# Kernel optimization log

Measured on AMD Instinct MI355X. Metric: run time of the kernel, lower is better.

## Reference

```python
import jax, jax.numpy as jnp
import numpy as np

N_NODES = 100000
N_HEDGES = 10000
D = 128  # i_d = v_d = e_d = q_d
NUM_CLASS = 10
E = 640000


def _linear_params(key, d_in, d_out):
    k1, k2 = jax.random.split(key)
    lim = 1.0 / np.sqrt(d_in)
    W = jax.random.uniform(k1, (d_in, d_out), jnp.float32, -lim, lim)
    b = jax.random.uniform(k2, (d_out,), jnp.float32, -lim, lim)
    return W, b


def setup_inputs() -> dict:
    key = jax.random.key(0)
    ks = jax.random.split(key, 12)
    vfeat = jax.random.normal(ks[0], (N_NODES, D), jnp.float32)
    efeat = jax.random.normal(ks[1], (N_HEDGES, D), jnp.float32)
    he_idx = jax.random.randint(ks[2], (E,), 0, N_HEDGES, jnp.int32)
    nd_idx = jax.random.randint(ks[3], (E,), 0, N_NODES, jnp.int32)
    Wfl, bfl = _linear_params(ks[4], D, D)   # first_layer_in: i_d -> v_d
    W1, b1 = _linear_params(ks[5], D, D)     # w1: e_d -> q_d
    W2, b2 = _linear_params(ks[6], D, D)     # w2: v_d -> q_d
    W3, b3 = _linear_params(ks[7], D, D)     # w3: v_d -> e_d
    W4, b4 = _linear_params(ks[8], D, D)     # w4: v_d -> q_d
    W5, b5 = _linear_params(ks[9], D, D)     # w5: e_d -> q_d
    W6, b6 = _linear_params(ks[10], D, D)    # w6: e_d -> v_d
    Wc, bc = _linear_params(ks[11], D, NUM_CLASS)
    return dict(vfeat=vfeat, efeat=efeat, he_idx=he_idx, nd_idx=nd_idx,
                first_layer=1, last_layer=1,
                Wfl=Wfl, bfl=bfl, W1=W1, b1=b1, W2=W2, b2=b2, W3=W3, b3=b3,
                W4=W4, b4=b4, W5=W5, b5=b5, W6=W6, b6=b6, Wc=Wc, bc=bc)


def _segment_softmax(logits, segs, num_segments):
    # softmax over the variable-size mailbox of each destination segment
    m = jax.ops.segment_max(logits, segs, num_segments=num_segments)
    m = jnp.where(jnp.isfinite(m), m, 0.0)  # empty segments
    e = jnp.exp(logits - m[segs])
    s = jax.ops.segment_sum(e, segs, num_segments=num_segments)
    return e / jnp.where(s > 0, s, 1.0)[segs]


def reference(vfeat, efeat, he_idx, nd_idx, first_layer, last_layer,
              Wfl, bfl, W1, b1, W2, b2, W3, b3, W4, b4, W5, b5, W6, b6, Wc, bc):
    scale = 1.0 / np.sqrt(D).astype(np.float32)
    # first_layer path (first_layer=1)
    feat_e = efeat @ Wfl + bfl                         # [M, v_d]
    k_e = feat_e @ W5 + b5                             # [M, q_d]
    v_e = feat_e @ W6 + b6                             # [M, v_d]
    q_v = vfeat @ W4 + b4                              # [N, q_d]
    # etype 'con': hyperedge -> node
    attn1 = jax.nn.leaky_relu((k_e[he_idx] * q_v[nd_idx]).sum(-1)) * scale  # [E]
    a1 = _segment_softmax(attn1, nd_idx, N_NODES)
    feat_v = jax.ops.segment_sum(a1[:, None] * v_e[he_idx], nd_idx,
                                 num_segments=N_NODES)  # [N, v_d]
    # etype 'in': node -> hyperedge
    k_v = feat_v @ W2 + b2                             # [N, q_d]
    v_v = feat_v @ W3 + b3                             # [N, e_d]
    q_e = feat_e @ W1 + b1                             # [M, q_d]
    attn2 = jax.nn.leaky_relu((k_v[nd_idx] * q_e[he_idx]).sum(-1)) * scale  # [E]
    a2 = _segment_softmax(attn2, he_idx, N_HEDGES)
    feat_e2 = jax.ops.segment_sum(a2[:, None] * v_v[nd_idx], he_idx,
                                  num_segments=N_HEDGES)  # [M, e_d]
    # last_layer path (last_layer=1): classification head (file save omitted)
    pred = feat_e2 @ Wc + bc                           # [M, num_class]
    return pred
```

## Files before the change

kernel.cpp:

```cpp
#include <hip/hip_runtime.h>
#include <hip/hip_bf16.h>
#include <math.h>


#define HY_M 10000
#define HY_N 100000
#define HY_E 640000

#define SH_N 9
#define NB_N 196
#define SH_M 6
#define NB_M 157

typedef float        f32x4 __attribute__((ext_vector_type(4)));
typedef unsigned int u32x4 __attribute__((ext_vector_type(4)));

__device__ __forceinline__ unsigned int f2bf(float x) {
    unsigned int u = __float_as_uint(x);
    return (u + 0x7fffu + ((u >> 16) & 1u)) >> 16;
}
__device__ __forceinline__ float2 bf2x2(unsigned int w) {
    float lo = __uint_as_float(w << 16);
    float hi = __uint_as_float(w & 0xffff0000u);
    return make_float2(lo, hi);
}
__device__ __forceinline__ float dot8(uint4 kw, float4 qa, float4 qb) {
    float2 k0 = bf2x2(kw.x), k1 = bf2x2(kw.y), k2 = bf2x2(kw.z), k3 = bf2x2(kw.w);
    return k0.x * qa.x + k0.y * qa.y + k1.x * qa.z + k1.y * qa.w
         + k2.x * qb.x + k2.y * qb.y + k3.x * qb.z + k3.y * qb.w;
}
__device__ __forceinline__ void unpack8(uint4 vw, float (&vf)[8]) {
    float2 v0 = bf2x2(vw.x), v1 = bf2x2(vw.y), v2 = bf2x2(vw.z), v3 = bf2x2(vw.w);
    vf[0] = v0.x; vf[1] = v0.y; vf[2] = v1.x; vf[3] = v1.y;
    vf[4] = v2.x; vf[5] = v2.y; vf[6] = v3.x; vf[7] = v3.y;
}

__global__ void zero_ints(int* __restrict__ p, int n) {
    int i = blockIdx.x * blockDim.x + threadIdx.x;
    if (i < n) p[i] = 0;
}

__launch_bounds__(256)
__global__ void coarse_hist(const int* __restrict__ nd, const int* __restrict__ he,
                            int* __restrict__ gcntN, int* __restrict__ gcntM, int E) {
    __shared__ int hN[256], hM[256];
    const int t = threadIdx.x;
    hN[t] = 0; hM[t] = 0;
    __syncthreads();
    const int base = blockIdx.x * 4096;
    for (int i = t; i < 4096; i += 256) {
        int e = base + i;
        if (e < E) {
            atomicAdd(&hN[nd[e] >> SH_N], 1);
            atomicAdd(&hM[he[e] >> SH_M], 1);
        }
    }
    __syncthreads();
    if (hN[t]) atomicAdd(&gcntN[t], hN[t]);
    if (hM[t]) atomicAdd(&gcntM[t], hM[t]);
}

__global__ void coarse_scan(const int* __restrict__ gcntN, const int* __restrict__ gcntM,
                            int* __restrict__ coffN, int* __restrict__ coffM, int E) {
    __shared__ int s[256];
    const int* g = blockIdx.x ? gcntM : gcntN;
    int* o = blockIdx.x ? coffM : coffN;
    const int nb = blockIdx.x ? NB_M : NB_N;
    const int t = threadIdx.x;
    int v = (t < nb) ? g[t] : 0;
    int orig = v;
    s[t] = v; __syncthreads();
    for (int off = 1; off < 256; off <<= 1) {
        int x = (t >= off) ? s[t - off] : 0;
        __syncthreads(); s[t] += x; __syncthreads();
    }
    if (t < nb) o[t] = s[t] - orig;
    if (t == 0) o[nb] = E;
}

__launch_bounds__(256)
__global__ void part_scatter(const int* __restrict__ nd, const int* __restrict__ he,
                             const int* __restrict__ coffN, const int* __restrict__ coffM,
                             int* __restrict__ gcurN, int* __restrict__ gcurM,
                             unsigned int* __restrict__ stN, unsigned int* __restrict__ stM,
                             int E) {
    __shared__ int hN[256], hM[256];
    const int t = threadIdx.x;
    hN[t] = 0; hM[t] = 0;
    __syncthreads();
    const int base = blockIdx.x * 4096;
    for (int i = t; i < 4096; i += 256) {
        int e = base + i;
        if (e < E) {
            atomicAdd(&hN[nd[e] >> SH_N], 1);
            atomicAdd(&hM[he[e] >> SH_M], 1);
        }
    }
    __syncthreads();
    int cN = hN[t], cM = hM[t];
    __syncthreads();
    if (cN) hN[t] = coffN[t] + atomicAdd(&gcurN[t], cN);
    if (cM) hM[t] = coffM[t] + atomicAdd(&gcurM[t], cM);
    __syncthreads();
    for (int i = t; i < 4096; i += 256) {
        int e = base + i;
        if (e < E) {
            int d = nd[e], h = he[e];
            int pN = atomicAdd(&hN[d >> SH_N], 1);
            stN[pN] = ((unsigned int)(d & 511) << 14) | (unsigned int)h;
            int pM = atomicAdd(&hM[h >> SH_M], 1);
            stM[pM] = ((unsigned int)(h & 63) << 17) | (unsigned int)d;
        }
    }
}

__launch_bounds__(256)
__global__ void bucket_build(const unsigned int* __restrict__ stN,
                             const unsigned int* __restrict__ stM,
                             const int* __restrict__ coffN, const int* __restrict__ coffM,
                             int* __restrict__ nd_off, int* __restrict__ he_off,
                             int* __restrict__ nd_adj, int* __restrict__ he_adj,
                             int* __restrict__ dcntg) {
    __shared__ int cnt[512];
    __shared__ int cur[512];
    __shared__ int ps[256];
    __shared__ int dh[64];
    int b = blockIdx.x;
    const int t = threadIdx.x;
    const unsigned int* st; const int* coff; int* offout; int* adj;
    int dmin, dcnt2, sshift; unsigned int smask; int ntot;
    const bool isN = b < NB_N;
    if (isN) {
        st = stN; coff = coffN; offout = nd_off; adj = nd_adj;
        dmin = b << SH_N; dcnt2 = min(512, HY_N - dmin);
        sshift = 14; smask = 0x3FFFu; ntot = HY_N;
    } else {
        b -= NB_N;
        st = stM; coff = coffM; offout = he_off; adj = he_adj;
        dmin = b << SH_M; dcnt2 = min(64, HY_M - dmin);
        sshift = 17; smask = 0x1FFFFu; ntot = HY_M;
    }
    const int cbase = coff[b], cend = coff[b + 1];
    cnt[t] = 0; cnt[t + 256] = 0;
    if (t < 64) dh[t] = 0;
    __syncthreads();
    for (int k = cbase + t; k < cend; k += 256)
        atomicAdd(&cnt[st[k] >> sshift], 1);
    __syncthreads();
    int a0 = cnt[2 * t], a1 = cnt[2 * t + 1];
    int pair = a0 + a1;
    ps[t] = pair;
    __syncthreads();
    for (int off = 1; off < 256; off <<= 1) {
        int x = (t >= off) ? ps[t - off] : 0;
        __syncthreads(); ps[t] += x; __syncthreads();
    }
    int excl = ps[t] - pair;
    cur[2 * t]     = cbase + excl;
    cur[2 * t + 1] = cbase + excl + a0;
    __syncthreads();
    for (int i = t; i < dcnt2; i += 256) offout[dmin + i] = cur[i];
    if (t == 0 && dmin + dcnt2 == ntot) offout[ntot] = cend;
    if (isN) {
        for (int i = t; i < dcnt2; i += 256)
            atomicAdd(&dh[min(cnt[i], 63)], 1);
    }
    __syncthreads();
    if (isN && t < 64 && dh[t]) atomicAdd(&dcntg[t], dh[t]);
    for (int k = cbase + t; k < cend; k += 256) {
        unsigned int w = st[k];
        int pos = atomicAdd(&cur[w >> sshift], 1);
        adj[pos] = (int)(w & smask);
    }
}

__global__ void deg_scan(const int* __restrict__ dcnt, int* __restrict__ dcur) {
    int t = threadIdx.x;
    int rt = 63 - t;
    int v = dcnt[rt];
    int s = v;
    for (int o = 1; o < 64; o <<= 1) {
        int x = __shfl_up(s, o, 64);
        if (t >= o) s += x;
    }
    dcur[rt] = s - v;
}

__launch_bounds__(256)
__global__ void deg_scatter(const int* __restrict__ off, int* __restrict__ dcur,
                            int* __restrict__ nperm, int n) {
    __shared__ int h[64];
    __shared__ int basev[64];
    int t = threadIdx.x;
    if (t < 64) h[t] = 0;
    __syncthreads();
    int i = blockIdx.x * blockDim.x + t;
    int bin = 0, lpos = 0;
    bool valid = i < n;
    if (valid) {
        bin = min(off[i + 1] - off[i], 63);
        lpos = atomicAdd(&h[bin], 1);
    }
    __syncthreads();
    if (t < 64 && h[t]) basev[t] = atomicAdd(&dcur[t], h[t]);
    __syncthreads();
    if (valid) nperm[basev[bin] + lpos] = i;
}

__device__ __forceinline__ void gemm_accum(const float* __restrict__ A,
        const float* __restrict__ W, int nrows, float* wlds,
        float (&acc)[4][4], int row0) {
    const int tid = threadIdx.x;
    const int cg = tid & 31;
    for (int i = tid; i < 4096; i += 512)
        ((float4*)wlds)[i] = ((const float4*)W)[i];
    __syncthreads();
    const float4* A0 = (const float4*)(A + (size_t)min(row0 + 0, nrows - 1) * 128);
    const float4* A1 = (const float4*)(A + (size_t)min(row0 + 1, nrows - 1) * 128);
    const float4* A2 = (const float4*)(A + (size_t)min(row0 + 2, nrows - 1) * 128);
    const float4* A3 = (const float4*)(A + (size_t)min(row0 + 3, nrows - 1) * 128);
    #pragma unroll 2
    for (int kq = 0; kq < 32; ++kq) {
        float4 ar[4] = {A0[kq], A1[kq], A2[kq], A3[kq]};
        const float4* wk = (const float4*)(wlds + kq * 512);
        float4 wr[4] = {wk[cg], wk[32 + cg], wk[64 + cg], wk[96 + cg]};
        #pragma unroll
        for (int r = 0; r < 4; ++r) {
            float av[4] = {ar[r].x, ar[r].y, ar[r].z, ar[r].w};
            #pragma unroll
            for (int j = 0; j < 4; ++j) {
                float wv[4] = {wr[j].x, wr[j].y, wr[j].z, wr[j].w};
                #pragma unroll
                for (int c = 0; c < 4; ++c)
                    acc[r][c] = fmaf(av[j], wv[c], acc[r][c]);
            }
        }
    }
}

__device__ __forceinline__ void gemm_store_f32(const float* __restrict__ b,
        float* __restrict__ Cf, int nrows, float (&acc)[4][4], int row0) {
    const int cg = threadIdx.x & 31;
    const float4 bv = ((const float4*)b)[cg];
    #pragma unroll
    for (int r = 0; r < 4; ++r) {
        int gr = row0 + r;
        if (gr < nrows) {
            float4 o = {acc[r][0] + bv.x, acc[r][1] + bv.y,
                        acc[r][2] + bv.z, acc[r][3] + bv.w};
            ((float4*)(Cf + (size_t)gr * 128))[cg] = o;
        }
    }
}

__launch_bounds__(512)
__global__ void gemm_pair(const float* __restrict__ Aa, const float* __restrict__ Wa,
                          float* __restrict__ Ca,
                          const float* __restrict__ Ab, const float* __restrict__ Wb,
                          float* __restrict__ Cb2, const float* __restrict__ zb) {
    __shared__ __align__(16) float wlds[16384];
    const int rs = threadIdx.x >> 5;
    const int row0 = blockIdx.x * 64 + rs * 4;
    const float* A = blockIdx.y ? Ab : Aa;
    const float* W = blockIdx.y ? Wb : Wa;
    float* C = blockIdx.y ? Cb2 : Ca;
    float acc[4][4] = {};
    gemm_accum(A, W, 128, wlds, acc, row0);
    gemm_store_f32(zb, C, 128, acc, row0);
}

__launch_bounds__(512)
__global__ void gemm_trip(const float* __restrict__ Wfl, const float* __restrict__ bfl,
        const float* __restrict__ W54, const float* __restrict__ b54v,
        const float* __restrict__ W6, const float* __restrict__ b6,
        const float* __restrict__ W12, const float* __restrict__ b12v,
        const float* __restrict__ w1b2, const float* __restrict__ s12,
        const float* __restrict__ w5b4, const float* __restrict__ s54,
        float* __restrict__ Wk, float* __restrict__ Wv, float* __restrict__ Wq,
        float* __restrict__ bk, float* __restrict__ bv, float* __restrict__ bq,
        float* __restrict__ u_c, float* __restrict__ u_k,
        float* __restrict__ t_c, float* __restrict__ t_k,
        const float* __restrict__ zb) {
    __shared__ __align__(16) float wlds[16384];
    const int y = blockIdx.y;
    if (y == 3) {
        if (blockIdx.x != 0) return;
        int t = threadIdx.x;
        if (t < 128) {
            float a1 = 0.f, a2 = 0.f, a3 = 0.f;
            for (int j = 0; j < 128; ++j) {
                float f = bfl[j];
                a1 += f * W54[j * 128 + t];
                a2 += f * W6[j * 128 + t];
                a3 += f * W12[j * 128 + t];
            }
            bk[t] = a1 + b54v[t];
            bv[t] = a2 + b6[t];
            bq[t] = a3 + b12v[t];
        } else if (t < 256) {
            int k = t - 128;
            float a1 = 0.f, a2 = 0.f;
            for (int j = 0; j < 128; ++j) {
                float f = Wfl[k * 128 + j];
                a1 += f * w1b2[j];
                a2 += f * w5b4[j];
            }
            u_c[k] = a1;
            u_k[k] = a2;
        }
        if (t == 0) {
            float a1 = 0.f, a2 = 0.f;
            for (int j = 0; j < 128; ++j) {
                a1 += bfl[j] * w1b2[j];
                a2 += bfl[j] * w5b4[j];
            }
            *t_c = a1 + *s12;
            *t_k = a2 + *s54;
        }
        return;
    }
    const int rs = threadIdx.x >> 5;
    const int row0 = blockIdx.x * 64 + rs * 4;
    const float* W = y == 0 ? W54 : (y == 1 ? W6 : W12);
    float* C = y == 0 ? Wk : (y == 1 ? Wv : Wq);
    float acc[4][4] = {};
    gemm_accum(Wfl, W, 128, wlds, acc, row0);
    gemm_store_f32(zb, C, 128, acc, row0);
}

__launch_bounds__(256)
__global__ void gemm_m(const float* __restrict__ A,
        const float* __restrict__ Wk, const float* __restrict__ bk,
        const float* __restrict__ Wv, const float* __restrict__ bvv,
        const float* __restrict__ Wq, const float* __restrict__ bq,
        unsigned short* __restrict__ kv, float* __restrict__ qt, int nrows) {
    __shared__ __align__(16) float wlds[128 * 64];
    const int tid = threadIdx.x;
    const int mat = blockIdx.y >> 1;
    const int half = blockIdx.y & 1;
    const float* W = mat == 0 ? Wk : (mat == 1 ? Wv : Wq);
    const float* bb = mat == 0 ? bk : (mat == 1 ? bvv : bq);
    const float4* W4 = (const float4*)W;
    float4* wl4 = (float4*)wlds;
    for (int i = tid; i < 2048; i += 256)
        wl4[i] = W4[(i >> 4) * 32 + half * 16 + (i & 15)];
    __syncthreads();
    const int cg = tid & 15;
    const int rs = tid >> 4;
    const int row0 = blockIdx.x * 32 + rs * 2;
    const float4* A0 = (const float4*)(A + (size_t)min(row0, nrows - 1) * 128);
    const float4* A1 = (const float4*)(A + (size_t)min(row0 + 1, nrows - 1) * 128);
    float acc[2][4] = {};
    #pragma unroll 4
    for (int kq = 0; kq < 32; ++kq) {
        float4 a0 = A0[kq], a1 = A1[kq];
        float av0[4] = {a0.x, a0.y, a0.z, a0.w};
        float av1[4] = {a1.x, a1.y, a1.z, a1.w};
        #pragma unroll
        for (int jj = 0; jj < 4; ++jj) {
            float4 w4 = wl4[(4 * kq + jj) * 16 + cg];
            float wv4[4] = {w4.x, w4.y, w4.z, w4.w};
            #pragma unroll
            for (int c = 0; c < 4; ++c) {
                acc[0][c] = fmaf(av0[jj], wv4[c], acc[0][c]);
                acc[1][c] = fmaf(av1[jj], wv4[c], acc[1][c]);
            }
        }
    }
    const float4 bv4 = ((const float4*)bb)[half * 16 + cg];
    #pragma unroll
    for (int r = 0; r < 2; ++r) {
        int gr = row0 + r;
        if (gr < nrows) {
            float o0 = acc[r][0] + bv4.x, o1 = acc[r][1] + bv4.y;
            float o2 = acc[r][2] + bv4.z, o3 = acc[r][3] + bv4.w;
            if (mat == 2) {
                float4 o = {o0, o1, o2, o3};
                ((float4*)(qt + (size_t)gr * 128))[half * 16 + cg] = o;
            } else {
                uint2 pk;
                pk.x = f2bf(o0) | (f2bf(o1) << 16);
                pk.y = f2bf(o2) | (f2bf(o3) << 16);
                *(uint2*)(kv + (size_t)gr * 256 + mat * 128 + half * 64 + cg * 4) = pk;
            }
        }
    }
}

__device__ __forceinline__ void prep_vecs_body(const float* WX, const float* WY,
        const float* bX, const float* bY, float* bXY, float* wXbY, float* sXY, int t) {
    if (t < 128) {
        float acc = 0.f;
        for (int j = 0; j < 128; ++j) acc += WY[t * 128 + j] * bX[j];
        bXY[t] = acc;
    } else {
        int k = t - 128;
        float acc = 0.f;
        for (int j = 0; j < 128; ++j) acc += WX[k * 128 + j] * bY[j];
        wXbY[k] = acc;
    }
    if (t == 0) {
        float acc = 0.f;
        for (int j = 0; j < 128; ++j) acc += bX[j] * bY[j];
        *sXY = acc;
    }
}

__global__ void prep_a(const float* __restrict__ W1, const float* __restrict__ b1,
                       const float* __restrict__ W2, const float* __restrict__ b2,
                       const float* __restrict__ W3, const float* __restrict__ b3,
                       const float* __restrict__ W4, const float* __restrict__ b4,
                       const float* __restrict__ W5, const float* __restrict__ b5,
                       const float* __restrict__ Wc,
                       float* __restrict__ W2T, float* __restrict__ W4T,
                       float* __restrict__ b12v, float* __restrict__ w1b2,
                       float* __restrict__ s12,
                       float* __restrict__ b54v, float* __restrict__ w5b4,
                       float* __restrict__ s54,
                       float* __restrict__ W3c, float* __restrict__ b3c,
                       float* __restrict__ zeros) {
    const int x = blockIdx.x, t = threadIdx.x;
    if (x < 64) {
        int i = x * 256 + t;
        W2T[(i & 127) * 128 + (i >> 7)] = W2[i];
    } else if (x < 128) {
        int i = (x - 64) * 256 + t;
        W4T[(i & 127) * 128 + (i >> 7)] = W4[i];
    } else if (x == 128) {
        prep_vecs_body(W1, W2, b1, b2, b12v, w1b2, s12, t);
    } else if (x == 129) {
        prep_vecs_body(W5, W4, b5, b4, b54v, w5b4, s54, t);
    } else if (x < 136) {
        int i = (x - 130) * 256 + t;
        if (i < 1280) {
            int k = i / 10, c = i % 10;
            float acc = 0.f;
            for (int j = 0; j < 128; ++j) acc += W3[k * 128 + j] * Wc[j * 10 + c];
            W3c[i] = acc;
        } else if (i < 1290) {
            int c = i - 1280;
            float acc = 0.f;
            for (int j = 0; j < 128; ++j) acc += b3[j] * Wc[j * 10 + c];
            b3c[c] = acc;
        }
    } else {
        if (t < 128) zeros[t] = 0.f;
    }
}

__launch_bounds__(256)
__global__ void dotc2(const float* __restrict__ X,
                      const float* __restrict__ u1, const float* __restrict__ t1v,
                      const float* __restrict__ u2, const float* __restrict__ t2v,
                      float* __restrict__ o1, float* __restrict__ o2, int M) {
    int w = (blockIdx.x * blockDim.x + threadIdx.x) >> 6;
    int lane = threadIdx.x & 63;
    if (w >= M) return;
    float2 r = ((const float2*)(X + (size_t)w * 128))[lane];
    float2 a1 = ((const float2*)u1)[lane];
    float2 a2 = ((const float2*)u2)[lane];
    float d1 = r.x * a1.x + r.y * a1.y;
    float d2 = r.x * a2.x + r.y * a2.y;
    #pragma unroll
    for (int o = 32; o; o >>= 1) {
        d1 += __shfl_xor(d1, o, 64);
        d2 += __shfl_xor(d2, o, 64);
    }
    if (lane == 0) { o1[w] = d1 + *t1v; o2[w] = d2 + *t2v; }
}

__launch_bounds__(256)
__global__ void attn_s1(const float* __restrict__ vf,
                        const unsigned int* __restrict__ kv,
                        const float* __restrict__ ck,
                        const int* __restrict__ off, const int* __restrict__ adj,
                        const int* __restrict__ nperm,
                        unsigned int* __restrict__ fv,
                        int nseg, float scale) {
    int slot = (blockIdx.x * blockDim.x + threadIdx.x) >> 4;
    int j = threadIdx.x & 15;
    if (slot >= nseg) return;
    int seg = nperm[slot];
    int beg = off[seg], end = off[seg + 1];
    const f32x4* qp = (const f32x4*)(vf + (size_t)seg * 128 + 8 * j);
    f32x4 qa4 = __builtin_nontemporal_load(qp);
    f32x4 qb4 = __builtin_nontemporal_load(qp + 1);
    float4 qa = {qa4.x, qa4.y, qa4.z, qa4.w};
    float4 qb = {qb4.x, qb4.y, qb4.z, qb4.w};
    float m = -INFINITY, l = 0.f;
    float a[8] = {};
    int i = beg;
    const int cnt = end - beg;
    if (cnt >= 2) {
        int s0 = adj[i], s1 = adj[i + 1];
        uint4 kw0 = ((const uint4*)(kv + (size_t)s0 * 128))[j];
        uint4 vw0 = ((const uint4*)(kv + (size_t)s0 * 128 + 64))[j];
        float c0 = ck[s0];
        uint4 kw1 = ((const uint4*)(kv + (size_t)s1 * 128))[j];
        uint4 vw1 = ((const uint4*)(kv + (size_t)s1 * 128 + 64))[j];
        float c1 = ck[s1];
        for (; i + 1 < end; i += 2) {
            uint4 ka = kw0, va = vw0, kb = kw1, vb = vw1;
            float ca = c0, cb = c1;
            if (i + 3 < end) {
                int t0 = adj[i + 2], t1 = adj[i + 3];
                kw0 = ((const uint4*)(kv + (size_t)t0 * 128))[j];
                vw0 = ((const uint4*)(kv + (size_t)t0 * 128 + 64))[j];
                c0 = ck[t0];
                kw1 = ((const uint4*)(kv + (size_t)t1 * 128))[j];
                vw1 = ((const uint4*)(kv + (size_t)t1 * 128 + 64))[j];
                c1 = ck[t1];
            } else if (i + 2 < end) {
                int t0 = adj[i + 2];
                kw0 = ((const uint4*)(kv + (size_t)t0 * 128))[j];
                vw0 = ((const uint4*)(kv + (size_t)t0 * 128 + 64))[j];
                c0 = ck[t0];
            }
            float d1 = dot8(ka, qa, qb);
            float d2 = dot8(kb, qa, qb);
            d1 += __shfl_xor(d1, 8); d2 += __shfl_xor(d2, 8);
            d1 += __shfl_xor(d1, 4); d2 += __shfl_xor(d2, 4);
            d1 += __shfl_xor(d1, 2); d2 += __shfl_xor(d2, 2);
            d1 += __shfl_xor(d1, 1); d2 += __shfl_xor(d2, 1);
            d1 += ca; d2 += cb;
            d1 = (d1 >= 0.f ? d1 : 0.01f * d1) * scale;
            d2 = (d2 >= 0.f ? d2 : 0.01f * d2) * scale;
            float mn = fmaxf(fmaxf(m, d1), d2);
            float r  = __expf(m - mn);
            float p1 = __expf(d1 - mn);
            float p2 = __expf(d2 - mn);
            l = l * r + p1 + p2;
            float v1[8], v2[8];
            unpack8(va, v1); unpack8(vb, v2);
            #pragma unroll
            for (int t = 0; t < 8; ++t)
                a[t] = fmaf(p2, v2[t], fmaf(p1, v1[t], a[t] * r));
            m = mn;
        }
        if (i < end) {
            float d = dot8(kw0, qa, qb);
            d += __shfl_xor(d, 8); d += __shfl_xor(d, 4);
            d += __shfl_xor(d, 2); d += __shfl_xor(d, 1);
            d += c0;
            d = (d >= 0.f ? d : 0.01f * d) * scale;
            float mn = fmaxf(m, d);
            float r = __expf(m - mn);
            float p = __expf(d - mn);
            l = l * r + p;
            float v1[8]; unpack8(vw0, v1);
            #pragma unroll
            for (int t = 0; t < 8; ++t)
                a[t] = fmaf(p, v1[t], a[t] * r);
            m = mn;
        }
    } else if (cnt == 1) {
        int s0 = adj[i];
        uint4 kw0 = ((const uint4*)(kv + (size_t)s0 * 128))[j];
        uint4 vw0 = ((const uint4*)(kv + (size_t)s0 * 128 + 64))[j];
        float d = dot8(kw0, qa, qb);
        d += __shfl_xor(d, 8); d += __shfl_xor(d, 4);
        d += __shfl_xor(d, 2); d += __shfl_xor(d, 1);
        d += ck[s0];
        d = (d >= 0.f ? d : 0.01f * d) * scale;
        l = 1.f;
        float v1[8]; unpack8(vw0, v1);
        #pragma unroll
        for (int t = 0; t < 8; ++t) a[t] = v1[t];
    }
    float inv = (l > 0.f) ? 1.f / l : 0.f;
    u32x4 o;
    o.x = f2bf(a[0] * inv) | (f2bf(a[1] * inv) << 16);
    o.y = f2bf(a[2] * inv) | (f2bf(a[3] * inv) << 16);
    o.z = f2bf(a[4] * inv) | (f2bf(a[5] * inv) << 16);
    o.w = f2bf(a[6] * inv) | (f2bf(a[7] * inv) << 16);
    __builtin_nontemporal_store(o, (u32x4*)(fv + (size_t)seg * 64 + 4 * j));
}

__launch_bounds__(256)
__global__ void attn_s2(const float* __restrict__ QT, const float* __restrict__ cvec,
                        const unsigned int* __restrict__ fv,
                        const int* __restrict__ off, const int* __restrict__ adj,
                        float* __restrict__ agg, float* __restrict__ flag, float scale) {
    __shared__ float sm[16], sl[16];
    __shared__ float sacc[16][16][9];
    const int seg = blockIdx.x;
    const int g = threadIdx.x >> 4;
    const int j = threadIdx.x & 15;
    const int beg = off[seg], end = off[seg + 1];
    const f32x4* qp = (const f32x4*)(QT + (size_t)seg * 128 + 8 * j);
    f32x4 qa4 = __builtin_nontemporal_load(qp);
    f32x4 qb4 = __builtin_nontemporal_load(qp + 1);
    float4 qa = {qa4.x, qa4.y, qa4.z, qa4.w};
    float4 qb = {qb4.x, qb4.y, qb4.z, qb4.w};
    const float cadd = cvec[seg];
    float m = -INFINITY, l = 0.f;
    float a[8] = {};
    int it = beg + g;
    if (it + 16 < end) {
        int s0 = adj[it], s1 = adj[it + 16];
        uint4 rw0 = ((const uint4*)(fv + (size_t)s0 * 64))[j];
        uint4 rw1 = ((const uint4*)(fv + (size_t)s1 * 64))[j];
        for (; it + 16 < end; it += 32) {
            uint4 ra = rw0, rb = rw1;
            if (it + 48 < end) {
                int t0 = adj[it + 32], t1 = adj[it + 48];
                rw0 = ((const uint4*)(fv + (size_t)t0 * 64))[j];
                rw1 = ((const uint4*)(fv + (size_t)t1 * 64))[j];
            } else if (it + 32 < end) {
                int t0 = adj[it + 32];
                rw0 = ((const uint4*)(fv + (size_t)t0 * 64))[j];
            }
            float v1[8], v2[8];
            unpack8(ra, v1); unpack8(rb, v2);
            float d1 = v1[0] * qa.x + v1[1] * qa.y + v1[2] * qa.z + v1[3] * qa.w
                     + v1[4] * qb.x + v1[5] * qb.y + v1[6] * qb.z + v1[7] * qb.w;
            float d2 = v2[0] * qa.x + v2[1] * qa.y + v2[2] * qa.z + v2[3] * qa.w
                     + v2[4] * qb.x + v2[5] * qb.y + v2[6] * qb.z + v2[7] * qb.w;
            d1 += __shfl_xor(d1, 8); d2 += __shfl_xor(d2, 8);
            d1 += __shfl_xor(d1, 4); d2 += __shfl_xor(d2, 4);
            d1 += __shfl_xor(d1, 2); d2 += __shfl_xor(d2, 2);
            d1 += __shfl_xor(d1, 1); d2 += __shfl_xor(d2, 1);
            d1 += cadd; d2 += cadd;
            d1 = (d1 >= 0.f ? d1 : 0.01f * d1) * scale;
            d2 = (d2 >= 0.f ? d2 : 0.01f * d2) * scale;
            float mn = fmaxf(fmaxf(m, d1), d2);
            float r  = __expf(m - mn);
            float p1 = __expf(d1 - mn);
            float p2 = __expf(d2 - mn);
            l = l * r + p1 + p2;
            #pragma unroll
            for (int t = 0; t < 8; ++t)
                a[t] = fmaf(p2, v2[t], fmaf(p1, v1[t], a[t] * r));
            m = mn;
        }
        if (it < end) {
            float v1[8]; unpack8(rw0, v1);
            float d = v1[0] * qa.x + v1[1] * qa.y + v1[2] * qa.z + v1[3] * qa.w
                    + v1[4] * qb.x + v1[5] * qb.y + v1[6] * qb.z + v1[7] * qb.w;
            d += __shfl_xor(d, 8); d += __shfl_xor(d, 4);
            d += __shfl_xor(d, 2); d += __shfl_xor(d, 1);
            d += cadd;
            d = (d >= 0.f ? d : 0.01f * d) * scale;
            float mn = fmaxf(m, d);
            float r = __expf(m - mn);
            float p = __expf(d - mn);
            l = l * r + p;
            #pragma unroll
            for (int t = 0; t < 8; ++t) a[t] = fmaf(p, v1[t], a[t] * r);
            m = mn;
        }
    } else if (it < end) {
        int s0 = adj[it];
        uint4 rw0 = ((const uint4*)(fv + (size_t)s0 * 64))[j];
        float v1[8]; unpack8(rw0, v1);
        float d = v1[0] * qa.x + v1[1] * qa.y + v1[2] * qa.z + v1[3] * qa.w
                + v1[4] * qb.x + v1[5] * qb.y + v1[6] * qb.z + v1[7] * qb.w;
        d += __shfl_xor(d, 8); d += __shfl_xor(d, 4);
        d += __shfl_xor(d, 2); d += __shfl_xor(d, 1);
        d += cadd;
        d = (d >= 0.f ? d : 0.01f * d) * scale;
        m = d; l = 1.f;
        #pragma unroll
        for (int t = 0; t < 8; ++t) a[t] = v1[t];
    }
    if (j == 0) { sm[g] = m; sl[g] = l; }
    #pragma unroll
    for (int t = 0; t < 8; ++t) sacc[g][j][t] = a[t];
    __syncthreads();
    if (threadIdx.x < 16) {
        float M2 = -INFINITY;
        #pragma unroll 4
        for (int gg = 0; gg < 16; ++gg) if (sl[gg] > 0.f) M2 = fmaxf(M2, sm[gg]);
        float L = 0.f;
        float acc[8] = {};
        #pragma unroll 4
        for (int gg = 0; gg < 16; ++gg) {
            float f = (sl[gg] > 0.f) ? __expf(sm[gg] - M2) : 0.f;
            L += f * sl[gg];
            #pragma unroll
            for (int t = 0; t < 8; ++t) acc[t] += f * sacc[gg][threadIdx.x][t];
        }
        float inv = (L > 0.f) ? 1.f / L : 0.f;
        f32x4 o1 = {acc[0] * inv, acc[1] * inv, acc[2] * inv, acc[3] * inv};
        f32x4 o2 = {acc[4] * inv, acc[5] * inv, acc[6] * inv, acc[7] * inv};
        f32x4* op = (f32x4*)(agg + (size_t)seg * 128 + 8 * threadIdx.x);
        __builtin_nontemporal_store(o1, op);
        __builtin_nontemporal_store(o2, op + 1);
        if (threadIdx.x == 0) flag[seg] = (L > 0.f) ? 1.f : 0.f;
    }
}

__global__ void head2(const float* __restrict__ agg, const float* __restrict__ flag,
                      const float* __restrict__ W3c, const float* __restrict__ b3c,
                      const float* __restrict__ bc, float* __restrict__ out, int M) {
    int t = blockIdx.x * blockDim.x + threadIdx.x;
    if (t >= M * 10) return;
    int row = t / 10, c = t % 10;
    float acc = bc[c] + flag[row] * b3c[c];
    #pragma unroll 8
    for (int k = 0; k < 128; ++k)
        acc = fmaf(agg[(size_t)row * 128 + k], W3c[k * 10 + c], acc);
    out[t] = acc;
}

extern "C" void kernel_launch(void* const* d_in, const int* in_sizes, int n_in,
                              void* d_out, int out_size, void* d_ws, size_t ws_size,
                              hipStream_t stream) {
    const float* vfeat = (const float*)d_in[0];
    const float* efeat = (const float*)d_in[1];
    const int*   he    = (const int*)d_in[2];
    const int*   nd    = (const int*)d_in[3];
    const float* Wfl = (const float*)d_in[6],  *bfl = (const float*)d_in[7];
    const float* W1  = (const float*)d_in[8],  *b1  = (const float*)d_in[9];
    const float* W2  = (const float*)d_in[10], *b2  = (const float*)d_in[11];
    const float* W3  = (const float*)d_in[12], *b3  = (const float*)d_in[13];
    const float* W4  = (const float*)d_in[14], *b4  = (const float*)d_in[15];
    const float* W5  = (const float*)d_in[16], *b5  = (const float*)d_in[17];
    const float* W6  = (const float*)d_in[18], *b6  = (const float*)d_in[19];
    const float* Wc  = (const float*)d_in[20], *bc  = (const float*)d_in[21];
    float* out = (float*)d_out;
    float* ws  = (float*)d_ws;

    const int M = HY_M, N = HY_N, E = HY_E;

    float* qt_e  = ws + 0;
    float* agg   = ws + 1280000;
    float* c_e   = ws + 2560000;
    float* ck    = ws + 2570000;
    float* flag  = ws + 2580000;
    float* W2T   = ws + 2590000;
    float* W4T   = ws + 2606384;
    float* W12   = ws + 2622768;
    float* W54   = ws + 2639152;
    float* Wk    = ws + 2655536;
    float* Wv    = ws + 2671920;
    float* Wq    = ws + 2688304;
    float* W3c   = ws + 2704688;
    float* b3c   = ws + 2705968;
    float* b12v  = ws + 2705984;
    float* w1b2  = ws + 2706112;
    float* s12   = ws + 2706240;
    float* b54v  = ws + 2706244;
    float* w5b4  = ws + 2706372;
    float* s54   = ws + 2706500;
    float* bk    = ws + 2706504;
    float* bv    = ws + 2706632;
    float* bq    = ws + 2706760;
    float* u_c   = ws + 2706888;
    float* u_k   = ws + 2707016;
    float* t_c   = ws + 2707144;
    float* t_k   = ws + 2707148;
    float* zeros = ws + 2707152;
    unsigned int* kv_bf = (unsigned int*)(ws + 2707280);
    unsigned int* fv_bf = kv_bf + (size_t)M * 128;
    int* nd_off = (int*)(fv_bf + (size_t)N * 64);
    int* he_off = nd_off + 100001;
    int* nd_adj = he_off + 10001;
    int* he_adj = nd_adj + 640000;
    int* nperm  = he_adj + 640000;
    unsigned int* stN = (unsigned int*)(nperm + 100000);
    unsigned int* stM = stN + 640000;
    int* gcntN = (int*)(stM + 640000);
    int* gcntM = gcntN + 256;
    int* gcurN = gcntM + 256;
    int* gcurM = gcurN + 256;
    int* dcnt  = gcurM + 256;
    int* dcur  = dcnt + 64;
    int* coffN = dcur + 64;
    int* coffM = coffN + 256;

    const float scale = 0.08838834764831843f;
    const int nchunk = (E + 4095) / 4096;

    zero_ints<<<5, 256, 0, stream>>>(gcntN, 1152);
    coarse_hist<<<nchunk, 256, 0, stream>>>(nd, he, gcntN, gcntM, E);
    coarse_scan<<<2, 256, 0, stream>>>(gcntN, gcntM, coffN, coffM, E);
    part_scatter<<<nchunk, 256, 0, stream>>>(nd, he, coffN, coffM,
                                             gcurN, gcurM, stN, stM, E);
    bucket_build<<<NB_N + NB_M, 256, 0, stream>>>(stN, stM, coffN, coffM,
                                                  nd_off, he_off, nd_adj, he_adj,
                                                  dcnt);
    deg_scan<<<1, 64, 0, stream>>>(dcnt, dcur);
    deg_scatter<<<(N + 255) / 256, 256, 0, stream>>>(nd_off, dcur, nperm, N);

    prep_a<<<137, 256, 0, stream>>>(W1, b1, W2, b2, W3, b3, W4, b4, W5, b5, Wc,
                                    W2T, W4T, b12v, w1b2, s12, b54v, w5b4, s54,
                                    W3c, b3c, zeros);
    gemm_pair<<<dim3(2, 2), 512, 0, stream>>>(W1, W2T, W12, W5, W4T, W54, zeros);
    gemm_trip<<<dim3(2, 4), 512, 0, stream>>>(Wfl, bfl, W54, b54v, W6, b6, W12, b12v,
                                              w1b2, s12, w5b4, s54,
                                              Wk, Wv, Wq, bk, bv, bq,
                                              u_c, u_k, t_c, t_k, zeros);

    gemm_m<<<dim3((M + 31) / 32, 6), 256, 0, stream>>>(
        efeat, Wk, bk, Wv, bv, Wq, bq, (unsigned short*)kv_bf, qt_e, M);
    dotc2<<<(M * 64 + 255) / 256, 256, 0, stream>>>(efeat, u_c, t_c, u_k, t_k,
                                                    c_e, ck, M);

    attn_s1<<<(N * 16 + 255) / 256, 256, 0, stream>>>(
        vfeat, kv_bf, ck, nd_off, nd_adj, nperm, fv_bf, N, scale);

    attn_s2<<<M, 256, 0, stream>>>(qt_e, c_e, fv_bf, he_off, he_adj, agg, flag, scale);

    head2<<<(M * 10 + 255) / 256, 256, 0, stream>>>(agg, flag, W3c, b3c, bc, out, M);
}
```

Before: 212.8 us.

## Fuse small kernels, shrink partition chunks, and unroll node attention by four

Several independent changes land together. The zeroing kernel is folded into prep_a, which now runs first. The dotc2 row-dot kernel becomes an extra grid slice of gemm_m, and the head classifier is fused into the attn_s2 epilogue, so the agg/flag buffers and two launches disappear. The histogram and scatter chunk size drops from 4096 to 1024 edges to get more blocks, and attn_s1 switches from a two-wide prefetching loop to a four-wide batched gather loop. These cut launch overhead and intermediate memory traffic, at the cost of more global atomics and losing the explicit software prefetch.

```diff
diff --git a/kernel.cpp b/kernel.cpp
--- a/kernel.cpp
+++ b/kernel.cpp
@@ -34,10 +34,10 @@
     vf[0] = v0.x; vf[1] = v0.y; vf[2] = v1.x; vf[3] = v1.y;
     vf[4] = v2.x; vf[5] = v2.y; vf[6] = v3.x; vf[7] = v3.y;
 }
-
-__global__ void zero_ints(int* __restrict__ p, int n) {
-    int i = blockIdx.x * blockDim.x + threadIdx.x;
-    if (i < n) p[i] = 0;
+__device__ __forceinline__ float red16(float d) {
+    d += __shfl_xor(d, 8); d += __shfl_xor(d, 4);
+    d += __shfl_xor(d, 2); d += __shfl_xor(d, 1);
+    return d;
 }
 
 __launch_bounds__(256)
@@ -47,8 +47,8 @@
     const int t = threadIdx.x;
     hN[t] = 0; hM[t] = 0;
     __syncthreads();
-    const int base = blockIdx.x * 4096;
-    for (int i = t; i < 4096; i += 256) {
+    const int base = blockIdx.x * 1024;
+    for (int i = t; i < 1024; i += 256) {
         int e = base + i;
         if (e < E) {
             atomicAdd(&hN[nd[e] >> SH_N], 1);
@@ -88,8 +88,8 @@
     const int t = threadIdx.x;
     hN[t] = 0; hM[t] = 0;
     __syncthreads();
-    const int base = blockIdx.x * 4096;
-    for (int i = t; i < 4096; i += 256) {
+    const int base = blockIdx.x * 1024;
+    for (int i = t; i < 1024; i += 256) {
         int e = base + i;
         if (e < E) {
             atomicAdd(&hN[nd[e] >> SH_N], 1);
@@ -102,7 +102,7 @@
     if (cN) hN[t] = coffN[t] + atomicAdd(&gcurN[t], cN);
     if (cM) hM[t] = coffM[t] + atomicAdd(&gcurM[t], cM);
     __syncthreads();
-    for (int i = t; i < 4096; i += 256) {
+    for (int i = t; i < 1024; i += 256) {
         int e = base + i;
         if (e < E) {
             int d = nd[e], h = he[e];
@@ -333,9 +333,32 @@
         const float* __restrict__ Wk, const float* __restrict__ bk,
         const float* __restrict__ Wv, const float* __restrict__ bvv,
         const float* __restrict__ Wq, const float* __restrict__ bq,
+        const float* __restrict__ u_c, const float* __restrict__ t_c,
+        const float* __restrict__ u_k, const float* __restrict__ t_k,
+        float* __restrict__ c_e, float* __restrict__ ck,
         unsigned short* __restrict__ kv, float* __restrict__ qt, int nrows) {
     __shared__ __align__(16) float wlds[128 * 64];
     const int tid = threadIdx.x;
+    if (blockIdx.y == 6) {
+        const int w = tid >> 6, lane = tid & 63;
+        float2 a1 = ((const float2*)u_c)[lane];
+        float2 a2 = ((const float2*)u_k)[lane];
+        for (int it = 0; it < 8; ++it) {
+            int row = blockIdx.x * 32 + it * 4 + w;
+            if (row < nrows) {
+                float2 r = ((const float2*)(A + (size_t)row * 128))[lane];
+                float d1 = r.x * a1.x + r.y * a1.y;
+                float d2 = r.x * a2.x + r.y * a2.y;
+                #pragma unroll
+                for (int o = 32; o; o >>= 1) {
+                    d1 += __shfl_xor(d1, o, 64);
+                    d2 += __shfl_xor(d2, o, 64);
+                }
+                if (lane == 0) { c_e[row] = d1 + *t_c; ck[row] = d2 + *t_k; }
+            }
+        }
+        return;
+    }
     const int mat = blockIdx.y >> 1;
     const int half = blockIdx.y & 1;
     const float* W = mat == 0 ? Wk : (mat == 1 ? Wv : Wq);
@@ -418,7 +441,7 @@
                        float* __restrict__ b54v, float* __restrict__ w5b4,
                        float* __restrict__ s54,
                        float* __restrict__ W3c, float* __restrict__ b3c,
-                       float* __restrict__ zeros) {
+                       float* __restrict__ zeros, int* __restrict__ zint) {
     const int x = blockIdx.x, t = threadIdx.x;
     if (x < 64) {
         int i = x * 256 + t;
@@ -443,30 +466,12 @@
             for (int j = 0; j < 128; ++j) acc += b3[j] * Wc[j * 10 + c];
             b3c[c] = acc;
         }
+    } else if (x == 136) {
+        if (t < 128) zeros[t] = 0.f;
     } else {
-        if (t < 128) zeros[t] = 0.f;
-    }
-}
-
-__launch_bounds__(256)
-__global__ void dotc2(const float* __restrict__ X,
-                      const float* __restrict__ u1, const float* __restrict__ t1v,
-                      const float* __restrict__ u2, const float* __restrict__ t2v,
-                      float* __restrict__ o1, float* __restrict__ o2, int M) {
-    int w = (blockIdx.x * blockDim.x + threadIdx.x) >> 6;
-    int lane = threadIdx.x & 63;
-    if (w >= M) return;
-    float2 r = ((const float2*)(X + (size_t)w * 128))[lane];
-    float2 a1 = ((const float2*)u1)[lane];
-    float2 a2 = ((const float2*)u2)[lane];
-    float d1 = r.x * a1.x + r.y * a1.y;
-    float d2 = r.x * a2.x + r.y * a2.y;
-    #pragma unroll
-    for (int o = 32; o; o >>= 1) {
-        d1 += __shfl_xor(d1, o, 64);
-        d2 += __shfl_xor(d2, o, 64);
-    }
-    if (lane == 0) { o1[w] = d1 + *t1v; o2[w] = d2 + *t2v; }
+        int i = (x - 137) * 256 + t;
+        if (i < 1152) zint[i] = 0;
+    }
 }
 
 __launch_bounds__(256)
@@ -490,82 +495,56 @@
     float m = -INFINITY, l = 0.f;
     float a[8] = {};
     int i = beg;
-    const int cnt = end - beg;
-    if (cnt >= 2) {
-        int s0 = adj[i], s1 = adj[i + 1];
-        uint4 kw0 = ((const uint4*)(kv + (size_t)s0 * 128))[j];
-        uint4 vw0 = ((const uint4*)(kv + (size_t)s0 * 128 + 64))[j];
-        float c0 = ck[s0];
-        uint4 kw1 = ((const uint4*)(kv + (size_t)s1 * 128))[j];
-        uint4 vw1 = ((const uint4*)(kv + (size_t)s1 * 128 + 64))[j];
-        float c1 = ck[s1];
-        for (; i + 1 < end; i += 2) {
-            uint4 ka = kw0, va = vw0, kb = kw1, vb = vw1;
-            float ca = c0, cb = c1;
-            if (i + 3 < end) {
-                int t0 = adj[i + 2], t1 = adj[i + 3];
-                kw0 = ((const uint4*)(kv + (size_t)t0 * 128))[j];
-                vw0 = ((const uint4*)(kv + (size_t)t0 * 128 + 64))[j];
-                c0 = ck[t0];
-                kw1 = ((const uint4*)(kv + (size_t)t1 * 128))[j];
-                vw1 = ((const uint4*)(kv + (size_t)t1 * 128 + 64))[j];
-                c1 = ck[t1];
-            } else if (i + 2 < end) {
-                int t0 = adj[i + 2];
-                kw0 = ((const uint4*)(kv + (size_t)t0 * 128))[j];
-                vw0 = ((const uint4*)(kv + (size_t)t0 * 128 + 64))[j];
-                c0 = ck[t0];
-            }
-            float d1 = dot8(ka, qa, qb);
-            float d2 = dot8(kb, qa, qb);
-            d1 += __shfl_xor(d1, 8); d2 += __shfl_xor(d2, 8);
-            d1 += __shfl_xor(d1, 4); d2 += __shfl_xor(d2, 4);
-            d1 += __shfl_xor(d1, 2); d2 += __shfl_xor(d2, 2);
-            d1 += __shfl_xor(d1, 1); d2 += __shfl_xor(d2, 1);
-            d1 += ca; d2 += cb;
-            d1 = (d1 >= 0.f ? d1 : 0.01f * d1) * scale;
-            d2 = (d2 >= 0.f ? d2 : 0.01f * d2) * scale;
-            float mn = fmaxf(fmaxf(m, d1), d2);
-            float r  = __expf(m - mn);
-            float p1 = __expf(d1 - mn);
-            float p2 = __expf(d2 - mn);
-            l = l * r + p1 + p2;
-            float v1[8], v2[8];
-            unpack8(va, v1); unpack8(vb, v2);
-            #pragma unroll
-            for (int t = 0; t < 8; ++t)
-                a[t] = fmaf(p2, v2[t], fmaf(p1, v1[t], a[t] * r));
-            m = mn;
-        }
-        if (i < end) {
-            float d = dot8(kw0, qa, qb);
-            d += __shfl_xor(d, 8); d += __shfl_xor(d, 4);
-            d += __shfl_xor(d, 2); d += __shfl_xor(d, 1);
-            d += c0;
-            d = (d >= 0.f ? d : 0.01f * d) * scale;
-            float mn = fmaxf(m, d);
-            float r = __expf(m - mn);
-            float p = __expf(d - mn);
-            l = l * r + p;
-            float v1[8]; unpack8(vw0, v1);
-            #pragma unroll
-            for (int t = 0; t < 8; ++t)
-                a[t] = fmaf(p, v1[t], a[t] * r);
-            m = mn;
-        }
-    } else if (cnt == 1) {
+    for (; i + 3 < end; i += 4) {
+        int s0 = adj[i], s1 = adj[i + 1], s2 = adj[i + 2], s3 = adj[i + 3];
+        const uint4* r0 = (const uint4*)(kv + (size_t)s0 * 128);
+        const uint4* r1 = (const uint4*)(kv + (size_t)s1 * 128);
+        const uint4* r2 = (const uint4*)(kv + (size_t)s2 * 128);
+        const uint4* r3 = (const uint4*)(kv + (size_t)s3 * 128);
+        uint4 k0 = r0[j], k1 = r1[j], k2 = r2[j], k3 = r3[j];
+        uint4 v0 = r0[16 + j], v1 = r1[16 + j], v2 = r2[16 + j], v3 = r3[16 + j];
+        float c0 = ck[s0], c1 = ck[s1], c2 = ck[s2], c3 = ck[s3];
+        float d0 = dot8(k0, qa, qb), d1 = dot8(k1, qa, qb);
+        float d2 = dot8(k2, qa, qb), d3 = dot8(k3, qa, qb);
+        #pragma unroll
+        for (int o = 8; o; o >>= 1) {
+            d0 += __shfl_xor(d0, o); d1 += __shfl_xor(d1, o);
+            d2 += __shfl_xor(d2, o); d3 += __shfl_xor(d3, o);
+        }
+        d0 += c0; d1 += c1; d2 += c2; d3 += c3;
+        d0 = (d0 >= 0.f ? d0 : 0.01f * d0) * scale;
+        d1 = (d1 >= 0.f ? d1 : 0.01f * d1) * scale;
+        d2 = (d2 >= 0.f ? d2 : 0.01f * d2) * scale;
+        d3 = (d3 >= 0.f ? d3 : 0.01f * d3) * scale;
+        float mn = fmaxf(fmaxf(fmaxf(d0, d1), fmaxf(d2, d3)), m);
+        float r  = __expf(m - mn);
+        float p0 = __expf(d0 - mn), p1 = __expf(d1 - mn);
+        float p2 = __expf(d2 - mn), p3 = __expf(d3 - mn);
+        l = l * r + p0 + p1 + p2 + p3;
+        float w0[8], w1[8], w2[8], w3[8];
+        unpack8(v0, w0); unpack8(v1, w1); unpack8(v2, w2); unpack8(v3, w3);
+        #pragma unroll
+        for (int t = 0; t < 8; ++t)
+            a[t] = fmaf(p3, w3[t], fmaf(p2, w2[t],
+                   fmaf(p1, w1[t], fmaf(p0, w0[t], a[t] * r))));
+        m = mn;
+    }
+    for (; i < end; ++i) {
         int s0 = adj[i];
-        uint4 kw0 = ((const uint4*)(kv + (size_t)s0 * 128))[j];
-        uint4 vw0 = ((const uint4*)(kv + (size_t)s0 * 128 + 64))[j];
-        float d = dot8(kw0, qa, qb);
-        d += __shfl_xor(d, 8); d += __shfl_xor(d, 4);
-        d += __shfl_xor(d, 2); d += __shfl_xor(d, 1);
+        const uint4* r0 = (const uint4*)(kv + (size_t)s0 * 128);
+        uint4 k0 = r0[j], v0 = r0[16 + j];
+        float d = dot8(k0, qa, qb);
+        d = red16(d);
         d += ck[s0];
         d = (d >= 0.f ? d : 0.01f * d) * scale;
-        l = 1.f;
-        float v1[8]; unpack8(vw0, v1);
-        #pragma unroll
-        for (int t = 0; t < 8; ++t) a[t] = v1[t];
+        float mn = fmaxf(m, d);
+        float r = __expf(m - mn);
+        float p = __expf(d - mn);
+        l = l * r + p;
+        float w0[8]; unpack8(v0, w0);
+        #pragma unroll
+        for (int t = 0; t < 8; ++t) a[t] = fmaf(p, w0[t], a[t] * r);
+        m = mn;
     }
     float inv = (l > 0.f) ? 1.f / l : 0.f;
     u32x4 o;
@@ -580,7 +559,9 @@
 __global__ void attn_s2(const float* __restrict__ QT, const float* __restrict__ cvec,
                         const unsigned int* __restrict__ fv,
                         const int* __restrict__ off, const int* __restrict__ adj,
-                        float* __restrict__ agg, float* __restrict__ flag, float scale) {
+                        const float* __restrict__ W3c, const float* __restrict__ b3c,
+                        const float* __restrict__ bc, float* __restrict__ out,
+                        float scale) {
     __shared__ float sm[16], sl[16];
     __shared__ float sacc[16][16][9];
     const int seg = blockIdx.x;
@@ -616,10 +597,8 @@
                      + v1[4] * qb.x + v1[5] * qb.y + v1[6] * qb.z + v1[7] * qb.w;
             float d2 = v2[0] * qa.x + v2[1] * qa.y + v2[2] * qa.z + v2[3] * qa.w
                      + v2[4] * qb.x + v2[5] * qb.y + v2[6] * qb.z + v2[7] * qb.w;
-            d1 += __shfl_xor(d1, 8); d2 += __shfl_xor(d2, 8);
-            d1 += __shfl_xor(d1, 4); d2 += __shfl_xor(d2, 4);
-            d1 += __shfl_xor(d1, 2); d2 += __shfl_xor(d2, 2);
-            d1 += __shfl_xor(d1, 1); d2 += __shfl_xor(d2, 1);
+            #pragma unroll
+            for (int o = 8; o; o >>= 1) { d1 += __shfl_xor(d1, o); d2 += __shfl_xor(d2, o); }
             d1 += cadd; d2 += cadd;
             d1 = (d1 >= 0.f ? d1 : 0.01f * d1) * scale;
             d2 = (d2 >= 0.f ? d2 : 0.01f * d2) * scale;
@@ -637,8 +616,7 @@
             float v1[8]; unpack8(rw0, v1);
             float d = v1[0] * qa.x + v1[1] * qa.y + v1[2] * qa.z + v1[3] * qa.w
                     + v1[4] * qb.x + v1[5] * qb.y + v1[6] * qb.z + v1[7] * qb.w;
-            d += __shfl_xor(d, 8); d += __shfl_xor(d, 4);
-            d += __shfl_xor(d, 2); d += __shfl_xor(d, 1);
+            d = red16(d);
             d += cadd;
             d = (d >= 0.f ? d : 0.01f * d) * scale;
             float mn = fmaxf(m, d);
@@ -655,8 +633,7 @@
         float v1[8]; unpack8(rw0, v1);
         float d = v1[0] * qa.x + v1[1] * qa.y + v1[2] * qa.z + v1[3] * qa.w
                 + v1[4] * qb.x + v1[5] * qb.y + v1[6] * qb.z + v1[7] * qb.w;
-        d += __shfl_xor(d, 8); d += __shfl_xor(d, 4);
-        d += __shfl_xor(d, 2); d += __shfl_xor(d, 1);
+        d = red16(d);
         d += cadd;
         d = (d >= 0.f ? d : 0.01f * d) * scale;
         m = d; l = 1.f;
@@ -668,6 +645,7 @@
     for (int t = 0; t < 8; ++t) sacc[g][j][t] = a[t];
     __syncthreads();
     if (threadIdx.x < 16) {
+        const int t16 = threadIdx.x;
         float M2 = -INFINITY;
         #pragma unroll 4
         for (int gg = 0; gg < 16; ++gg) if (sl[gg] > 0.f) M2 = fmaxf(M2, sm[gg]);
@@ -678,29 +656,32 @@
             float f = (sl[gg] > 0.f) ? __expf(sm[gg] - M2) : 0.f;
             L += f * sl[gg];
             #pragma unroll
-            for (int t = 0; t < 8; ++t) acc[t] += f * sacc[gg][threadIdx.x][t];
+            for (int t = 0; t < 8; ++t) acc[t] += f * sacc[gg][t16][t];
         }
         float inv = (L > 0.f) ? 1.f / L : 0.f;
-        f32x4 o1 = {acc[0] * inv, acc[1] * inv, acc[2] * inv, acc[3] * inv};
-        f32x4 o2 = {acc[4] * inv, acc[5] * inv, acc[6] * inv, acc[7] * inv};
-        f32x4* op = (f32x4*)(agg + (size_t)seg * 128 + 8 * threadIdx.x);
-        __builtin_nontemporal_store(o1, op);
-        __builtin_nontemporal_store(o2, op + 1);
-        if (threadIdx.x == 0) flag[seg] = (L > 0.f) ? 1.f : 0.f;
-    }
-}
-
-__global__ void head2(const float* __restrict__ agg, const float* __restrict__ flag,
-                      const float* __restrict__ W3c, const float* __restrict__ b3c,
-                      const float* __restrict__ bc, float* __restrict__ out, int M) {
-    int t = blockIdx.x * blockDim.x + threadIdx.x;
-    if (t >= M * 10) return;
-    int row = t / 10, c = t % 10;
-    float acc = bc[c] + flag[row] * b3c[c];
-    #pragma unroll 8
-    for (int k = 0; k < 128; ++k)
-        acc = fmaf(agg[(size_t)row * 128 + k], W3c[k * 10 + c], acc);
-    out[t] = acc;
+        float fl  = (L > 0.f) ? 1.f : 0.f;
+        #pragma unroll
+        for (int t = 0; t < 8; ++t) acc[t] *= inv;
+        float pp[10];
+        #pragma unroll
+        for (int c = 0; c < 10; ++c) {
+            float s = 0.f;
+            #pragma unroll
+            for (int t = 0; t < 8; ++t)
+                s = fmaf(acc[t], W3c[(8 * t16 + t) * 10 + c], s);
+            pp[c] = s;
+        }
+        #pragma unroll
+        for (int o = 8; o; o >>= 1) {
+            #pragma unroll
+            for (int c = 0; c < 10; ++c) pp[c] += __shfl_xor(pp[c], o);
+        }
+        if (t16 == 0) {
+            #pragma unroll
+            for (int c = 0; c < 10; ++c)
+                out[(size_t)seg * 10 + c] = pp[c] + fl * b3c[c] + bc[c];
+        }
+    }
 }
 
 extern "C" void kernel_launch(void* const* d_in, const int* in_sizes, int n_in,
@@ -724,34 +705,32 @@
     const int M = HY_M, N = HY_N, E = HY_E;
 
     float* qt_e  = ws + 0;
-    float* agg   = ws + 1280000;
-    float* c_e   = ws + 2560000;
-    float* ck    = ws + 2570000;
-    float* flag  = ws + 2580000;
-    float* W2T   = ws + 2590000;
-    float* W4T   = ws + 2606384;
-    float* W12   = ws + 2622768;
-    float* W54   = ws + 2639152;
-    float* Wk    = ws + 2655536;
-    float* Wv    = ws + 2671920;
-    float* Wq    = ws + 2688304;
-    float* W3c   = ws + 2704688;
-    float* b3c   = ws + 2705968;
-    float* b12v  = ws + 2705984;
-    float* w1b2  = ws + 2706112;
-    float* s12   = ws + 2706240;
-    float* b54v  = ws + 2706244;
-    float* w5b4  = ws + 2706372;
-    float* s54   = ws + 2706500;
-    float* bk    = ws + 2706504;
-    float* bv    = ws + 2706632;
-    float* bq    = ws + 2706760;
-    float* u_c   = ws + 2706888;
-    float* u_k   = ws + 2707016;
-    float* t_c   = ws + 2707144;
-    float* t_k   = ws + 2707148;
-    float* zeros = ws + 2707152;
-    unsigned int* kv_bf = (unsigned int*)(ws + 2707280);
+    float* c_e   = ws + 1280000;
+    float* ck    = ws + 1290000;
+    float* W2T   = ws + 1300000;
+    float* W4T   = ws + 1316384;
+    float* W12   = ws + 1332768;
+    float* W54   = ws + 1349152;
+    float* Wk    = ws + 1365536;
+    float* Wv    = ws + 1381920;
+    float* Wq    = ws + 1398304;
+    float* W3c   = ws + 1414688;
+    float* b3c   = ws + 1415968;
+    float* b12v  = ws + 1415984;
+    float* w1b2  = ws + 1416112;
+    float* s12   = ws + 1416240;
+    float* b54v  = ws + 1416244;
+    float* w5b4  = ws + 1416372;
+    float* s54   = ws + 1416500;
+    float* bk    = ws + 1416504;
+    float* bv    = ws + 1416632;
+    float* bq    = ws + 1416760;
+    float* u_c   = ws + 1416888;
+    float* u_k   = ws + 1417016;
+    float* t_c   = ws + 1417144;
+    float* t_k   = ws + 1417148;
+    float* zeros = ws + 1417152;
+    unsigned int* kv_bf = (unsigned int*)(ws + 1417280);
     unsigned int* fv_bf = kv_bf + (size_t)M * 128;
     int* nd_off = (int*)(fv_bf + (size_t)N * 64);
     int* he_off = nd_off + 100001;
@@ -770,9 +749,12 @@
     int* coffM = coffN + 256;
 
     const float scale = 0.08838834764831843f;
-    const int nchunk = (E + 4095) / 4096;
-
-    zero_ints<<<5, 256, 0, stream>>>(gcntN, 1152);
+    const int nchunk = (E + 1023) / 1024;
+
+    prep_a<<<142, 256, 0, stream>>>(W1, b1, W2, b2, W3, b3, W4, b4, W5, b5, Wc,
+                                    W2T, W4T, b12v, w1b2, s12, b54v, w5b4, s54,
+                                    W3c, b3c, zeros, gcntN);
+
     coarse_hist<<<nchunk, 256, 0, stream>>>(nd, he, gcntN, gcntM, E);
     coarse_scan<<<2, 256, 0, stream>>>(gcntN, gcntM, coffN, coffM, E);
     part_scatter<<<nchunk, 256, 0, stream>>>(nd, he, coffN, coffM,
@@ -783,24 +765,19 @@
     deg_scan<<<1, 64, 0, stream>>>(dcnt, dcur);
     deg_scatter<<<(N + 255) / 256, 256, 0, stream>>>(nd_off, dcur, nperm, N);
 
-    prep_a<<<137, 256, 0, stream>>>(W1, b1, W2, b2, W3, b3, W4, b4, W5, b5, Wc,
-                                    W2T, W4T, b12v, w1b2, s12, b54v, w5b4, s54,
-                                    W3c, b3c, zeros);
     gemm_pair<<<dim3(2, 2), 512, 0, stream>>>(W1, W2T, W12, W5, W4T, W54, zeros);
     gemm_trip<<<dim3(2, 4), 512, 0, stream>>>(Wfl, bfl, W54, b54v, W6, b6, W12, b12v,
                                               w1b2, s12, w5b4, s54,
                                               Wk, Wv, Wq, bk, bv, bq,
                                               u_c, u_k, t_c, t_k, zeros);
 
-    gemm_m<<<dim3((M + 31) / 32, 6), 256, 0, stream>>>(
-        efeat, Wk, bk, Wv, bv, Wq, bq, (unsigned short*)kv_bf, qt_e, M);
-    dotc2<<<(M * 64 + 255) / 256, 256, 0, stream>>>(efeat, u_c, t_c, u_k, t_k,
-                                                    c_e, ck, M);
+    gemm_m<<<dim3((M + 31) / 32, 7), 256, 0, stream>>>(
+        efeat, Wk, bk, Wv, bv, Wq, bq, u_c, t_c, u_k, t_k, c_e, ck,
+        (unsigned short*)kv_bf, qt_e, M);
 
     attn_s1<<<(N * 16 + 255) / 256, 256, 0, stream>>>(
         vfeat, kv_bf, ck, nd_off, nd_adj, nperm, fv_bf, N, scale);
 
-    attn_s2<<<M, 256, 0, stream>>>(qt_e, c_e, fv_bf, he_off, he_adj, agg, flag, scale);
-
-    head2<<<(M * 10 + 255) / 256, 256, 0, stream>>>(agg, flag, W3c, b3c, bc, out, M);
-}
+    attn_s2<<<M, 256, 0, stream>>>(qt_e, c_e, fv_bf, he_off, he_adj,
+                                   W3c, b3c, bc, out, scale);
+}
```

After: 215.7 us. About the same (+1.4%).
